# Optimization experiments

Hardware: AMD Instinct MI355X
Metric: run time of the kernel (lower is better)

The kernel has to match this reference:

```python
import jax, jax.numpy as jnp
import numpy as np
from jax import lax


def fake_quant_w(w):
    # Brevitas Int8WeightPerTensorFloat-style: per-tensor symmetric int8 fake quant
    scale = jnp.max(jnp.abs(w)) / 127.0
    wq = jnp.clip(jnp.round(w / scale), -128.0, 127.0) * scale
    return w + lax.stop_gradient(wq - w)


def conv(x, w, b, groups):
    y = lax.conv_general_dilated(
        x, w,
        window_strides=(1, 1),
        padding='SAME' if w.shape[-1] == 3 else 'VALID',
        dimension_numbers=('NCHW', 'OIHW', 'NCHW'),
        feature_group_count=groups,
    )
    return y + b[None, :, None, None]


def setup_inputs() -> dict:
    key = jax.random.key(0)
    ks = jax.random.split(key, 9)
    B, C_in, C_hid, H, W = 16, 128, 256, 64, 128
    x = jax.random.normal(ks[0], (B, C_in, H, W), dtype=jnp.float32)
    # depthwise conv1: groups=C_in, OIHW = [C_in, 1, 3, 3]
    dw1 = jax.random.normal(ks[1], (C_in, 1, 3, 3), dtype=jnp.float32) * 0.1
    db1 = jax.random.normal(ks[2], (C_in,), dtype=jnp.float32) * 0.01
    # pointwise conv1: [C_hid, C_in, 1, 1]
    pw1 = jax.random.normal(ks[3], (C_hid, C_in, 1, 1), dtype=jnp.float32) * 0.05
    pb1 = jax.random.normal(ks[4], (C_hid,), dtype=jnp.float32) * 0.01
    # depthwise conv2: [C_hid, 1, 3, 3]
    dw2 = jax.random.normal(ks[5], (C_hid, 1, 3, 3), dtype=jnp.float32) * 0.1
    db2 = jax.random.normal(ks[6], (C_hid,), dtype=jnp.float32) * 0.01
    # pointwise conv2: [2, C_hid, 1, 1]
    pw2 = jax.random.normal(ks[7], (2, C_hid, 1, 1), dtype=jnp.float32) * 0.05
    pb2 = jax.random.normal(ks[8], (2,), dtype=jnp.float32) * 0.01
    return {'x': x, 'dw1': dw1, 'db1': db1, 'pw1': pw1, 'pb1': pb1,
            'dw2': dw2, 'db2': db2, 'pw2': pw2, 'pb2': pb2}


def reference(x, dw1, db1, pw1, pb1, dw2, db2, pw2, pb2):
    C_in = x.shape[1]
    C_hid = pw1.shape[0]
    h = conv(x, fake_quant_w(dw1), db1, groups=C_in)      # depthwise 3x3
    h = conv(h, fake_quant_w(pw1), pb1, groups=1)          # pointwise -> C_hid
    h = jax.nn.relu(h)
    h = conv(h, fake_quant_w(dw2), db2, groups=C_hid)      # depthwise 3x3
    out = conv(h, fake_quant_w(pw2), pb2, groups=1)        # pointwise -> 2
    return out
```

## Files before the change

### kernel.cpp

```cpp
#include <hip/hip_runtime.h>
#include <math.h>

#define C_IN  128
#define C_HID 256
#define HGT   64
#define WID   128
#define NBATCH 16
#define HW (HGT * WID)

typedef unsigned int   uint32;
typedef unsigned short u16;
typedef float f32x4  __attribute__((ext_vector_type(4)));
typedef short bf16x8 __attribute__((ext_vector_type(8)));

__device__ __forceinline__ uint32 f2bf_bits(float f) {
    uint32 u = __float_as_uint(f);
    u = (u + 0x7fff + ((u >> 16) & 1)) >> 16;
    return u;
}
__device__ __forceinline__ float qclip(float v) {
    return fminf(fmaxf(v, -128.0f), 127.0f);
}

__global__ __launch_bounds__(1024) void quant4_kernel(
    const float* __restrict__ dw1, const float* __restrict__ pw1,
    const float* __restrict__ dw2, const float* __restrict__ pw2,
    const float* __restrict__ db2,
    float* __restrict__ qdw1T, u16* __restrict__ Blin,
    u16* __restrict__ W18lin, float* __restrict__ scales)
{
    const float* w; int n;
    switch (blockIdx.x) {
        case 0:  w = dw1; n = C_IN * 9;    break;
        case 1:  w = pw1; n = C_HID * C_IN; break;
        case 2:  w = dw2; n = C_HID * 9;   break;
        default: w = pw2; n = 2 * C_HID;   break;
    }
    __shared__ float sm[1024];
    int tid = threadIdx.x;
    const f32x4* w4 = (const f32x4*)w;
    int n4 = n >> 2;
    float m = 0.0f;
    #pragma unroll 4
    for (int i = tid; i < n4; i += 1024) {
        f32x4 v = w4[i];
        m = fmaxf(m, fmaxf(fmaxf(fabsf(v.x), fabsf(v.y)),
                           fmaxf(fabsf(v.z), fabsf(v.w))));
    }
    sm[tid] = m;
    __syncthreads();
    for (int s = 512; s > 0; s >>= 1) {
        if (tid < s) sm[tid] = fmaxf(sm[tid], sm[tid + s]);
        __syncthreads();
    }
    const float scale = sm[0] / 127.0f;

    if (blockIdx.x == 0) {
        for (int i = tid; i < C_IN * 9; i += 1024) {
            int t = i >> 7, cin = i & 127;
            float v = qclip(rintf(dw1[cin * 9 + t] / scale));
            qdw1T[i] = v * scale;
        }
    } else if (blockIdx.x == 1) {
        if (tid == 0) scales[0] = scale;
        #pragma unroll
        for (int i = tid; i < 4096; i += 1024) {
            int kstep = i >> 10;
            int cf    = (i >> 6) & 15;
            int l     = i & 63;
            int co    = cf * 16 + (l & 15);
            int k0    = kstep * 32 + ((l >> 4) << 3);
            const float* src = pw1 + (size_t)co * C_IN + k0;
            f32x4 a = *(const f32x4*)src;
            f32x4 b = *(const f32x4*)(src + 4);
            float vv[8] = {a.x, a.y, a.z, a.w, b.x, b.y, b.z, b.w};
            uint32 pk[4];
            #pragma unroll
            for (int p = 0; p < 4; ++p) {
                float v0 = qclip(rintf(vv[2 * p]     / scale));
                float v1 = qclip(rintf(vv[2 * p + 1] / scale));
                pk[p] = f2bf_bits(v0) | (f2bf_bits(v1) << 16);
            }
            ((uint4*)Blin)[i] = make_uint4(pk[0], pk[1], pk[2], pk[3]);
        }
    } else if (blockIdx.x == 2) {
    } else {
        const float s_p = scale;
        __syncthreads();

        const f32x4* d4 = (const f32x4*)dw2;
        float md = 0.0f;
        for (int i = tid; i < 576; i += 1024) {
            f32x4 v = d4[i];
            md = fmaxf(md, fmaxf(fmaxf(fabsf(v.x), fabsf(v.y)),
                                 fmaxf(fabsf(v.z), fabsf(v.w))));
        }
        sm[tid] = md;
        __syncthreads();
        for (int s = 512; s > 0; s >>= 1) {
            if (tid < s) sm[tid] = fmaxf(sm[tid], sm[tid + s]);
            __syncthreads();
        }
        const float s_d = sm[0] / 127.0f;

        {
            int ks  = tid >> 7;
            int jt  = (tid >> 6) & 1;
            int l   = tid & 63;
            int j   = jt * 16 + (l & 15);
            int ch0 = ks * 32 + ((l >> 4) << 3);
            uint32 pk[4] = {0, 0, 0, 0};
            if (j < 18) {
                int t9 = j >> 1, o = j & 1;
                float wv[8];
                #pragma unroll
                for (int p = 0; p < 8; ++p) {
                    int ch = ch0 + p;
                    float qd = qclip(rintf(dw2[ch * 9 + t9] / s_d)) * s_d;
                    float qp = qclip(rintf(pw2[o * C_HID + ch] / s_p)) * s_p;
                    wv[p] = qd * qp;
                }
                #pragma unroll
                for (int p = 0; p < 4; ++p)
                    pk[p] = f2bf_bits(wv[2 * p]) | (f2bf_bits(wv[2 * p + 1]) << 16);
            }
            ((uint4*)W18lin)[tid] = make_uint4(pk[0], pk[1], pk[2], pk[3]);
        }

        #pragma unroll
        for (int o = 0; o < 2; ++o) {
            __syncthreads();
            if (tid < 256) {
                float qv = qclip(rintf(pw2[o * C_HID + tid] / s_p)) * s_p;
                sm[tid] = qv * db2[tid];
            }
            __syncthreads();
            for (int s = 128; s > 0; s >>= 1) {
                if (tid < s) sm[tid] += sm[tid + s];
                __syncthreads();
            }
            if (tid == 0) scales[1 + o] = sm[0];
        }
    }
}

__global__ __launch_bounds__(512, 4) void fused_main(
    const float* __restrict__ x,
    const float* __restrict__ qdw1T, const float* __restrict__ db1,
    const u16* __restrict__ Blin, const float* __restrict__ pb1,
    const u16* __restrict__ W18lin,
    const float* __restrict__ scales,
    float* __restrict__ Mg)
{
    __shared__ __align__(16) unsigned char smem_raw[64 * 264 * 2];
    __shared__ float Ml[18][66];
    u16 (*h1s)[140]  = (u16 (*)[140])smem_raw;
    u16 (*h2pm)[264] = (u16 (*)[264])smem_raw;

    const int bid = blockIdx.x;
    const int swz = (bid & 7) * 256 + (bid >> 3);
    const int nb  = swz >> 7;
    const int y   = (swz >> 1) & 63;
    const int xh  = swz & 1;
    const int pxb0 = xh << 6;
    const int tid = threadIdx.x;
    const int wave = tid >> 6, lane = tid & 63;

    {
        const int q = tid & 15, g = tid >> 4;
        const int px0 = q << 2, cin0 = g << 2;

        f32x4 bia = *(const f32x4*)(db1 + cin0);
        float a32[4][4];
        #pragma unroll
        for (int c = 0; c < 4; ++c)
            #pragma unroll
            for (int p = 0; p < 4; ++p) a32[c][p] = ((const float*)&bia)[c];

        #pragma unroll
        for (int ky = 0; ky < 3; ++ky) {
            int yy = y + ky - 1;
            if (yy < 0 || yy >= HGT) continue;
            const float* rowbase = x + (((size_t)nb * C_IN + cin0) * HGT + yy) * WID + pxb0;

            f32x4 mid[4];
            #pragma unroll
            for (int c = 0; c < 4; ++c)
                mid[c] = *(const f32x4*)(rowbase + (size_t)c * HW + px0);

            float w3[3][4];
            #pragma unroll
            for (int kx = 0; kx < 3; ++kx) {
                f32x4 wv = *(const f32x4*)(qdw1T + (ky * 3 + kx) * C_IN + cin0);
                w3[kx][0] = wv.x; w3[kx][1] = wv.y; w3[kx][2] = wv.z; w3[kx][3] = wv.w;
            }

            #pragma unroll
            for (int c = 0; c < 4; ++c) {
                const float* rowc = rowbase + (size_t)c * HW;
                float lf = __shfl_up(mid[c].w, 1);
                float rt = __shfl_down(mid[c].x, 1);
                if (q == 0)  lf = xh        ? rowc[px0 - 1] : 0.0f;
                if (q == 15) rt = (xh == 0) ? rowc[px0 + 4] : 0.0f;
                float seg[6] = {lf, mid[c].x, mid[c].y, mid[c].z, mid[c].w, rt};
                #pragma unroll
                for (int kx = 0; kx < 3; ++kx)
                    #pragma unroll
                    for (int p = 0; p < 4; ++p)
                        a32[c][p] = fmaf(w3[kx][c], seg[p + kx], a32[c][p]);
            }
        }

        #pragma unroll
        for (int p = 0; p < 4; ++p) {
            uint2 pk;
            pk.x = f2bf_bits(a32[0][p]) | (f2bf_bits(a32[1][p]) << 16);
            pk.y = f2bf_bits(a32[2][p]) | (f2bf_bits(a32[3][p]) << 16);
            *(uint2*)&h1s[px0 + p][cin0] = pk;
        }
    }
    __syncthreads();

    const int l15 = lane & 15, l4 = lane >> 4;
    const int pxt = wave & 3;
    const int coh = wave >> 2;
    const int px0w = pxt << 4;
    const float bscale = scales[0];

    f32x4 acc[8];
    #pragma unroll
    for (int c = 0; c < 8; ++c) acc[c] = f32x4{0, 0, 0, 0};

    const bf16x8* BL = (const bf16x8*)Blin;

    #pragma unroll
    for (int ks = 0; ks < 4; ++ks) {
        bf16x8 afrag = *(const bf16x8*)&h1s[px0w + l15][ks * 32 + l4 * 8];
        #pragma unroll
        for (int c = 0; c < 8; ++c) {
            bf16x8 bfrag = BL[(ks * 16 + coh * 8 + c) * 64 + lane];
            acc[c] = __builtin_amdgcn_mfma_f32_16x16x32_bf16(afrag, bfrag, acc[c], 0, 0, 0);
        }
    }

    __syncthreads();

    #pragma unroll
    for (int c = 0; c < 8; ++c) {
        int co = coh * 128 + c * 16 + l15;
        int pxb = px0w + l4 * 4;
        float bias = pb1[co];
        #pragma unroll
        for (int i = 0; i < 4; ++i) {
            float v = fmaxf(fmaf(acc[c][i], bscale, bias), 0.0f);
            h2pm[pxb + i][co] = (u16)f2bf_bits(v);
        }
    }
    __syncthreads();

    {
        const int pxt3 = wave & 3;
        const int jt   = wave >> 2;
        const int px0t = pxt3 << 4;
        const bf16x8* WL = (const bf16x8*)W18lin;

        f32x4 acc2 = f32x4{0, 0, 0, 0};
        #pragma unroll 2
        for (int ks = 0; ks < 8; ++ks) {
            bf16x8 af = *(const bf16x8*)&h2pm[px0t + l15][ks * 32 + l4 * 8];
            bf16x8 bf = WL[(ks * 2 + jt) * 64 + lane];
            acc2 = __builtin_amdgcn_mfma_f32_16x16x32_bf16(af, bf, acc2, 0, 0, 0);
        }

        int j = jt * 16 + l15;
        if (j < 18) {
            #pragma unroll
            for (int i = 0; i < 4; ++i)
                Ml[j][px0t + l4 * 4 + i] = acc2[i];
        }
    }
    __syncthreads();

    {
        float* base = Mg + (size_t)swz * (18 * 64);
        for (int t = tid; t < 18 * 64; t += 512)
            base[t] = Ml[t >> 6][t & 63];
    }
}

__global__ __launch_bounds__(512) void gather_out(
    const float* __restrict__ Mg, const float* __restrict__ pb2,
    const float* __restrict__ scales, float* __restrict__ out)
{
    int idx = blockIdx.x * 512 + threadIdx.x;
    int px = idx & 127;
    int yy = (idx >> 7) & 63;
    int o  = (idx >> 13) & 1;
    int nb = idx >> 14;
    float v = pb2[o] + scales[1 + o];
    #pragma unroll
    for (int ky = 0; ky < 3; ++ky) {
        int z = yy + ky - 1;
        if (z < 0 || z >= HGT) continue;
        #pragma unroll
        for (int kx = 0; kx < 3; ++kx) {
            int pxs = px + kx - 1;
            if (pxs < 0 || pxs >= WID) continue;
            int xh2 = pxs >> 6, px2 = pxs & 63;
            int j = (ky * 3 + kx) * 2 + o;
            v += Mg[((size_t)(((nb * 64 + z) << 1) + xh2) * 18 + j) * 64 + px2];
        }
    }
    out[idx] = v;
}

extern "C" void kernel_launch(void* const* d_in, const int* in_sizes, int n_in,
                              void* d_out, int out_size, void* d_ws, size_t ws_size,
                              hipStream_t stream) {
    const float* x   = (const float*)d_in[0];
    const float* dw1 = (const float*)d_in[1];
    const float* db1 = (const float*)d_in[2];
    const float* pw1 = (const float*)d_in[3];
    const float* pb1 = (const float*)d_in[4];
    const float* dw2 = (const float*)d_in[5];
    const float* db2 = (const float*)d_in[6];
    const float* pw2 = (const float*)d_in[7];
    const float* pb2 = (const float*)d_in[8];
    float* out = (float*)d_out;

    char* wsb = (char*)d_ws;
    u16*   Blin   = (u16*)wsb;
    float* qdw1T  = (float*)(wsb + 65536);
    float* scales = (float*)(wsb + 65536 + 4608);
    u16*   W18lin = (u16*)(wsb + 65536 + 4608 + 64);
    float* Mg     = (float*)(wsb + 98304);

    quant4_kernel<<<4, 1024, 0, stream>>>(dw1, pw1, dw2, pw2, db2,
                                          qdw1T, Blin, W18lin, scales);

    fused_main<<<NBATCH * HGT * 2, 512, 0, stream>>>(
        x, qdw1T, db1, Blin, pb1, W18lin, scales, Mg);

    gather_out<<<512, 512, 0, stream>>>(Mg, pb2, scales, out);
}
```

Measured before the change: 56.81 us.

## Process full image rows per block and fold horizontal taps before global write

Each block now covers a full 128-pixel row with 1024 threads instead of a 64-pixel half-row with 512. This removes the cross-half halo loads from global memory and the duplicated per-block weight fetches. The block also sums the three kx taps in shared memory before writing, so the intermediate buffer shrinks from 18 to 6 values per pixel and the gather kernel reads 3 values per output instead of up to 9. In exchange the block needs more shared memory and the grid has half as many, larger blocks, which may lower occupancy.

```diff
diff --git a/kernel.cpp b/kernel.cpp
--- a/kernel.cpp
+++ b/kernel.cpp
@@ -144,30 +144,28 @@
     }
 }
 
-__global__ __launch_bounds__(512, 4) void fused_main(
+__global__ __launch_bounds__(1024, 8) void fused_main(
     const float* __restrict__ x,
     const float* __restrict__ qdw1T, const float* __restrict__ db1,
     const u16* __restrict__ Blin, const float* __restrict__ pb1,
     const u16* __restrict__ W18lin,
     const float* __restrict__ scales,
-    float* __restrict__ Mg)
+    float* __restrict__ Pg)
 {
-    __shared__ __align__(16) unsigned char smem_raw[64 * 264 * 2];
-    __shared__ float Ml[18][66];
-    u16 (*h1s)[140]  = (u16 (*)[140])smem_raw;
+    __shared__ __align__(16) unsigned char smem_raw[C_HID * 132 * 2];
+    __shared__ float Ml[128][20];
+    u16 (*h1s)[136]  = (u16 (*)[136])smem_raw;
     u16 (*h2pm)[264] = (u16 (*)[264])smem_raw;
 
     const int bid = blockIdx.x;
-    const int swz = (bid & 7) * 256 + (bid >> 3);
-    const int nb  = swz >> 7;
-    const int y   = (swz >> 1) & 63;
-    const int xh  = swz & 1;
-    const int pxb0 = xh << 6;
+    const int swz = (bid & 7) * 128 + (bid >> 3);
+    const int nb  = swz >> 6;
+    const int y   = swz & 63;
     const int tid = threadIdx.x;
     const int wave = tid >> 6, lane = tid & 63;
 
     {
-        const int q = tid & 15, g = tid >> 4;
+        const int q = tid & 31, g = tid >> 5;
         const int px0 = q << 2, cin0 = g << 2;
 
         f32x4 bia = *(const f32x4*)(db1 + cin0);
@@ -181,12 +179,12 @@
         for (int ky = 0; ky < 3; ++ky) {
             int yy = y + ky - 1;
             if (yy < 0 || yy >= HGT) continue;
-            const float* rowbase = x + (((size_t)nb * C_IN + cin0) * HGT + yy) * WID + pxb0;
+            const float* xbase = x + (((size_t)nb * C_IN + cin0) * HGT + yy) * WID;
 
             f32x4 mid[4];
             #pragma unroll
             for (int c = 0; c < 4; ++c)
-                mid[c] = *(const f32x4*)(rowbase + (size_t)c * HW + px0);
+                mid[c] = *(const f32x4*)(xbase + (size_t)c * HW + px0);
 
             float w3[3][4];
             #pragma unroll
@@ -197,11 +195,10 @@
 
             #pragma unroll
             for (int c = 0; c < 4; ++c) {
-                const float* rowc = rowbase + (size_t)c * HW;
                 float lf = __shfl_up(mid[c].w, 1);
                 float rt = __shfl_down(mid[c].x, 1);
-                if (q == 0)  lf = xh        ? rowc[px0 - 1] : 0.0f;
-                if (q == 15) rt = (xh == 0) ? rowc[px0 + 4] : 0.0f;
+                lf = (q > 0)  ? lf : 0.0f;
+                rt = (q < 31) ? rt : 0.0f;
                 float seg[6] = {lf, mid[c].x, mid[c].y, mid[c].z, mid[c].w, rt};
                 #pragma unroll
                 for (int kx = 0; kx < 3; ++kx)
@@ -222,9 +219,9 @@
     __syncthreads();
 
     const int l15 = lane & 15, l4 = lane >> 4;
-    const int pxt = wave & 3;
-    const int coh = wave >> 2;
-    const int px0w = pxt << 4;
+    const int wpx = wave & 7;
+    const int wco = wave >> 3;
+    const int px0w = wpx << 4;
     const float bscale = scales[0];
 
     f32x4 acc[8];
@@ -238,7 +235,7 @@
         bf16x8 afrag = *(const bf16x8*)&h1s[px0w + l15][ks * 32 + l4 * 8];
         #pragma unroll
         for (int c = 0; c < 8; ++c) {
-            bf16x8 bfrag = BL[(ks * 16 + coh * 8 + c) * 64 + lane];
+            bf16x8 bfrag = BL[(ks * 16 + wco * 8 + c) * 64 + lane];
             acc[c] = __builtin_amdgcn_mfma_f32_16x16x32_bf16(afrag, bfrag, acc[c], 0, 0, 0);
         }
     }
@@ -247,7 +244,7 @@
 
     #pragma unroll
     for (int c = 0; c < 8; ++c) {
-        int co = coh * 128 + c * 16 + l15;
+        int co = wco * 128 + c * 16 + l15;
         int pxb = px0w + l4 * 4;
         float bias = pb1[co];
         #pragma unroll
@@ -259,8 +256,8 @@
     __syncthreads();
 
     {
-        const int pxt3 = wave & 3;
-        const int jt   = wave >> 2;
+        const int pxt3 = wave & 7;
+        const int jt   = wave >> 3;
         const int px0t = pxt3 << 4;
         const bf16x8* WL = (const bf16x8*)W18lin;
 
@@ -276,20 +273,27 @@
         if (j < 18) {
             #pragma unroll
             for (int i = 0; i < 4; ++i)
-                Ml[j][px0t + l4 * 4 + i] = acc2[i];
-        }
-    }
-    __syncthreads();
-
-    {
-        float* base = Mg + (size_t)swz * (18 * 64);
-        for (int t = tid; t < 18 * 64; t += 512)
-            base[t] = Ml[t >> 6][t & 63];
+                Ml[px0t + l4 * 4 + i][j] = acc2[i];
+        }
+    }
+    __syncthreads();
+
+    if (tid < 768) {
+        int r = tid >> 7, px = tid & 127;
+        int ky = r >> 1, o = r & 1;
+        float v = 0.0f;
+        #pragma unroll
+        for (int kx = 0; kx < 3; ++kx) {
+            int pxs = px + kx - 1;
+            if (pxs >= 0 && pxs < WID)
+                v += Ml[pxs][(ky * 3 + kx) * 2 + o];
+        }
+        Pg[((size_t)(nb * HGT + y) * 6 + r) * WID + px] = v;
     }
 }
 
 __global__ __launch_bounds__(512) void gather_out(
-    const float* __restrict__ Mg, const float* __restrict__ pb2,
+    const float* __restrict__ Pg, const float* __restrict__ pb2,
     const float* __restrict__ scales, float* __restrict__ out)
 {
     int idx = blockIdx.x * 512 + threadIdx.x;
@@ -301,15 +305,8 @@
     #pragma unroll
     for (int ky = 0; ky < 3; ++ky) {
         int z = yy + ky - 1;
-        if (z < 0 || z >= HGT) continue;
-        #pragma unroll
-        for (int kx = 0; kx < 3; ++kx) {
-            int pxs = px + kx - 1;
-            if (pxs < 0 || pxs >= WID) continue;
-            int xh2 = pxs >> 6, px2 = pxs & 63;
-            int j = (ky * 3 + kx) * 2 + o;
-            v += Mg[((size_t)(((nb * 64 + z) << 1) + xh2) * 18 + j) * 64 + px2];
-        }
+        if (z >= 0 && z < HGT)
+            v += Pg[((size_t)(nb * HGT + z) * 6 + ky * 2 + o) * WID + px];
     }
     out[idx] = v;
 }
@@ -333,13 +330,13 @@
     float* qdw1T  = (float*)(wsb + 65536);
     float* scales = (float*)(wsb + 65536 + 4608);
     u16*   W18lin = (u16*)(wsb + 65536 + 4608 + 64);
-    float* Mg     = (float*)(wsb + 98304);
+    float* Pg     = (float*)(wsb + 98304);
 
     quant4_kernel<<<4, 1024, 0, stream>>>(dw1, pw1, dw2, pw2, db2,
                                           qdw1T, Blin, W18lin, scales);
 
-    fused_main<<<NBATCH * HGT * 2, 512, 0, stream>>>(
-        x, qdw1T, db1, Blin, pb1, W18lin, scales, Mg);
-
-    gather_out<<<512, 512, 0, stream>>>(Mg, pb2, scales, out);
-}
+    fused_main<<<NBATCH * HGT, 1024, 0, stream>>>(
+        x, qdw1T, db1, Blin, pb1, W18lin, scales, Pg);
+
+    gather_out<<<512, 512, 0, stream>>>(Pg, pb2, scales, out);
+}
```

Measured after the change: 55.83 us. No clear change (-1.7%).
